# Performance work log

Measured on AMD Instinct MI355X. Metric: run time of the kernel, lower is better.

## Reference

```python
import jax, jax.numpy as jnp
import numpy as np

NUM_NODES = 50000
NUM_HYPEREDGES = 10000
NUM_INCIDENCES = 800000
CHANNELS = 256
NEG_SLOPE = 0.01  # torch leaky_relu default negative_slope


def setup_inputs() -> dict:
    key = jax.random.key(0)
    k_n, k_e, k_emb, k_cw, k_lw, k_lb = jax.random.split(key, 6)
    node_idx = jax.random.randint(k_n, (NUM_INCIDENCES,), 0, NUM_NODES, dtype=jnp.int32)
    edge_idx = jax.random.randint(k_e, (NUM_INCIDENCES,), 0, NUM_HYPEREDGES, dtype=jnp.int32)
    edge_index = jnp.stack([node_idx, edge_idx], axis=0)  # [2, nnz] incidence list
    s = 1.0 / np.sqrt(CHANNELS).astype(np.float32)
    emb = jax.random.normal(k_emb, (NUM_NODES, CHANNELS), jnp.float32)  # Node2Vec embedding table
    conv_w = jax.random.normal(k_cw, (CHANNELS, CHANNELS), jnp.float32) * s  # HypergraphConv.lin (no bias)
    conv_b = jnp.zeros((CHANNELS,), jnp.float32)  # HypergraphConv.bias
    lin_w = jax.random.normal(k_lw, (CHANNELS, CHANNELS), jnp.float32) * s
    lin_b = jax.random.normal(k_lb, (CHANNELS,), jnp.float32) * s
    return {"emb": emb, "conv_w": conv_w, "conv_b": conv_b,
            "lin_w": lin_w, "lin_b": lin_b, "edge_index": edge_index}


def reference(emb, conv_w, conv_b, lin_w, lin_b, edge_index):
    node_idx, edge_idx = edge_index[0], edge_index[1]
    # HypergraphConv (use_attention=False): X' = D^-1 H B^-1 H^T (X W^T) + b
    x = emb @ conv_w.T  # [N, C]
    ones = jnp.ones((NUM_INCIDENCES,), x.dtype)
    D = jax.ops.segment_sum(ones, node_idx, num_segments=NUM_NODES)       # node degree
    Dinv = jnp.where(D > 0, 1.0 / D, 0.0)
    B = jax.ops.segment_sum(ones, edge_idx, num_segments=NUM_HYPEREDGES)  # hyperedge degree
    Binv = jnp.where(B > 0, 1.0 / B, 0.0)
    # node -> hyperedge aggregation
    e = jax.ops.segment_sum(x[node_idx], edge_idx, num_segments=NUM_HYPEREDGES) * Binv[:, None]  # [E, C]
    # hyperedge -> node aggregation
    n = jax.ops.segment_sum(e[edge_idx], node_idx, num_segments=NUM_NODES) * Dinv[:, None] + conv_b  # [N, C]
    y = jax.nn.leaky_relu(n, NEG_SLOPE)
    g = y.T @ y  # [C, C] Gram
    out = jax.nn.leaky_relu(g @ lin_w.T + lin_b, NEG_SLOPE)
    return out
```

## Files before the change

### kernel.cpp

```cpp
#include <hip/hip_runtime.h>

#define N_NODES 50000
#define N_EDGES 10000
#define NNZ     800000
#define C       256
#define SLOPE   0.01f
#define KTOT    50176
#define KCHUNK  512
#define NZB     98
#define MPAD    10048
#define NHALF   25000

#define NB      250
#define EB_E    40
#define EB_N    200
#define CHUNK   3125
#define CAP     6000
#define MP_E    288
#define MP_N    1408

#define EAGG_G  314
#define NAGG_G  1568

#define OFF_CC_E    0
#define OFF_CC_N    1024
#define OFF_CUR_E   2048
#define OFF_CUR_N   3072
#define OFF_DEG_E   4096
#define OFF_DEG_N   45056
#define ZERO_BYTES  245760
#define OFF_CB_E    266240
#define OFF_CB_N    267264
#define OFF_RS_N    268288
#define OFF_RS_E    468480
#define OFF_BUF_E   508672
#define OFF_BUF_N   3708672
#define OFF_CSR_E   6908672
#define OFF_CSR_N   10108672
#define OFF_EMBH    13308672
#define OFF_YT      13308672
#define OFF_E2      44144640
#define OFF_CWH     49289216
#define OFF_PART    49420288
#define OFF_EACCP   OFF_PART

typedef __attribute__((ext_vector_type(8))) short short8;
typedef __attribute__((ext_vector_type(4))) float floatx4;

static __device__ __forceinline__ unsigned short f2bf(float f) {
    unsigned int u = __float_as_uint(f);
    u = (u + 0x7fffu + ((u >> 16) & 1u)) >> 16;
    return (unsigned short)u;
}

static __device__ __forceinline__ void acc_bf8(const uint4 d, float* a) {
    a[0] += __uint_as_float(d.x << 16);
    a[1] += __uint_as_float(d.x & 0xffff0000u);
    a[2] += __uint_as_float(d.y << 16);
    a[3] += __uint_as_float(d.y & 0xffff0000u);
    a[4] += __uint_as_float(d.z << 16);
    a[5] += __uint_as_float(d.z & 0xffff0000u);
    a[6] += __uint_as_float(d.w << 16);
    a[7] += __uint_as_float(d.w & 0xffff0000u);
}

static __device__ __forceinline__ void idx8(const uint4 pk, int* ix) {
    ix[0] = (int)(pk.x & 0xffffu); ix[1] = (int)(pk.x >> 16);
    ix[2] = (int)(pk.y & 0xffffu); ix[3] = (int)(pk.y >> 16);
    ix[4] = (int)(pk.z & 0xffffu); ix[5] = (int)(pk.z >> 16);
    ix[6] = (int)(pk.w & 0xffffu); ix[7] = (int)(pk.w >> 16);
}

static __device__ __forceinline__ unsigned bfadd2(unsigned x, unsigned y) {
    float lx = __uint_as_float(x << 16), hx = __uint_as_float(x & 0xffff0000u);
    float ly = __uint_as_float(y << 16), hy = __uint_as_float(y & 0xffff0000u);
    return (unsigned)f2bf(lx + ly) | ((unsigned)f2bf(hx + hy) << 16);
}
static __device__ __forceinline__ uint4 bfadd8(uint4 x, uint4 y) {
    x.x = bfadd2(x.x, y.x); x.y = bfadd2(x.y, y.y);
    x.z = bfadd2(x.z, y.z); x.w = bfadd2(x.w, y.w);
    return x;
}

__global__ __launch_bounds__(256) void zero_kernel(float4* __restrict__ p, int n4) {
    int i = blockIdx.x * 256 + threadIdx.x;
    if (i < n4) p[i] = make_float4(0.f, 0.f, 0.f, 0.f);
}

#define PREP_EMB_BLOCKS 6251
#define PREP_CW_BLOCKS  32
__global__ __launch_bounds__(256) void prep_kernel(const float4* __restrict__ emb4,
                                                   uint4* __restrict__ embh4,
                                                   const float4* __restrict__ cw4,
                                                   uint4* __restrict__ cwh4,
                                                   const int* __restrict__ node_idx,
                                                   const int* __restrict__ edge_idx,
                                                   int* __restrict__ cc_e,
                                                   int* __restrict__ cc_n) {
    __shared__ int he[NB], hn[NB];
    int b = blockIdx.x, tid = threadIdx.x;
    if (b < PREP_EMB_BLOCKS) {
        int i = b * 256 + tid;
        if (i >= 1600032) return;
        uint4 o = {0u, 0u, 0u, 0u};
        if (i < 1600000) {
            float4 f0 = emb4[2 * i], f1 = emb4[2 * i + 1];
            o.x = f2bf(f0.x) | ((unsigned)f2bf(f0.y) << 16);
            o.y = f2bf(f0.z) | ((unsigned)f2bf(f0.w) << 16);
            o.z = f2bf(f1.x) | ((unsigned)f2bf(f1.y) << 16);
            o.w = f2bf(f1.z) | ((unsigned)f2bf(f1.w) << 16);
        }
        int node = i >> 5, c = i & 31;
        embh4[((size_t)(c >> 3) * 50001 + node) * 8 + (c & 7)] = o;
    } else if (b < PREP_EMB_BLOCKS + PREP_CW_BLOCKS) {
        int i = (b - PREP_EMB_BLOCKS) * 256 + tid;
        float4 f0 = cw4[2 * i], f1 = cw4[2 * i + 1];
        uint4 o;
        o.x = f2bf(f0.x) | ((unsigned)f2bf(f0.y) << 16);
        o.y = f2bf(f0.z) | ((unsigned)f2bf(f0.w) << 16);
        o.z = f2bf(f1.x) | ((unsigned)f2bf(f1.y) << 16);
        o.w = f2bf(f1.z) | ((unsigned)f2bf(f1.w) << 16);
        cwh4[i] = o;
    } else {
        int base = (b - PREP_EMB_BLOCKS - PREP_CW_BLOCKS) * CHUNK;
        for (int i = tid; i < NB; i += 256) { he[i] = 0; hn[i] = 0; }
        __syncthreads();
        for (int i = tid; i < CHUNK; i += 256) {
            atomicAdd(&he[edge_idx[base + i] / EB_E], 1);
            atomicAdd(&hn[node_idx[base + i] / EB_N], 1);
        }
        __syncthreads();
        for (int k = tid; k < NB; k += 256) {
            if (he[k]) atomicAdd(&cc_e[k], he[k]);
            if (hn[k]) atomicAdd(&cc_n[k], hn[k]);
        }
    }
}

__global__ __launch_bounds__(256) void coarse_scan_kernel(const int* __restrict__ cc_e,
                                                          const int* __restrict__ cc_n,
                                                          int* __restrict__ cb_e,
                                                          int* __restrict__ cb_n) {
    __shared__ int tmp[256];
    int tid = threadIdx.x;
    int v = (tid < NB) ? cc_e[tid] : 0;
    tmp[tid] = v;
    __syncthreads();
    for (int off = 1; off < 256; off <<= 1) {
        int t = (tid >= off) ? tmp[tid - off] : 0;
        __syncthreads();
        tmp[tid] += t;
        __syncthreads();
    }
    if (tid < NB) cb_e[tid + 1] = tmp[tid];
    if (tid == 0) cb_e[0] = 0;
    __syncthreads();
    v = (tid < NB) ? cc_n[tid] : 0;
    tmp[tid] = v;
    __syncthreads();
    for (int off = 1; off < 256; off <<= 1) {
        int t = (tid >= off) ? tmp[tid - off] : 0;
        __syncthreads();
        tmp[tid] += t;
        __syncthreads();
    }
    if (tid < NB) cb_n[tid + 1] = tmp[tid];
    if (tid == 0) cb_n[0] = 0;
}

__global__ __launch_bounds__(256) void bucket_scatter_kernel(const int* __restrict__ node_idx,
                                                             const int* __restrict__ edge_idx,
                                                             const int* __restrict__ cb_e,
                                                             const int* __restrict__ cb_n,
                                                             int* __restrict__ cur_e,
                                                             int* __restrict__ cur_n,
                                                             int* __restrict__ buf_e,
                                                             int* __restrict__ buf_n) {
    __shared__ int he[NB], hn[NB], be[NB], bn[NB];
    int tid = threadIdx.x;
    int base = blockIdx.x * CHUNK;
    for (int i = tid; i < NB; i += 256) { he[i] = 0; hn[i] = 0; }
    __syncthreads();
    int pe[13], pn[13];
    #pragma unroll
    for (int k = 0; k < 13; k++) {
        int i = tid + k * 256;
        if (i < CHUNK) {
            int e = edge_idx[base + i], v = node_idx[base + i];
            int ke = e / EB_E, kn = v / EB_N;
            pe[k] = (ke << 12) | atomicAdd(&he[ke], 1);
            pn[k] = (kn << 12) | atomicAdd(&hn[kn], 1);
        }
    }
    __syncthreads();
    for (int k = tid; k < NB; k += 256) {
        int c = he[k];
        be[k] = cb_e[k] + (c ? atomicAdd(&cur_e[k], c) : 0);
        int cn = hn[k];
        bn[k] = cb_n[k] + (cn ? atomicAdd(&cur_n[k], cn) : 0);
    }
    __syncthreads();
    #pragma unroll
    for (int k = 0; k < 13; k++) {
        int i = tid + k * 256;
        if (i < CHUNK) {
            int e = edge_idx[base + i], v = node_idx[base + i];
            int ke = pe[k] >> 12, oe = pe[k] & 4095;
            buf_e[be[ke] + oe] = (v << 6) | (e - ke * EB_E);
            int kn = pn[k] >> 12, on = pn[k] & 4095;
            buf_n[bn[kn] + on] = (e << 8) | (v - kn * EB_N);
        }
    }
}

__global__ __launch_bounds__(256) void bucket_sort_kernel(const int* __restrict__ buf_e,
                                                          const int* __restrict__ buf_n,
                                                          const int* __restrict__ cb_e,
                                                          const int* __restrict__ cb_n,
                                                          unsigned short* __restrict__ csr_e,
                                                          unsigned short* __restrict__ csr_n,
                                                          int* __restrict__ rs_e,
                                                          int* __restrict__ rs_n,
                                                          int* __restrict__ deg_e,
                                                          int* __restrict__ deg_n) {
    __shared__ int A[CAP];
    __shared__ int h[EB_N], bs[EB_N], cs[EB_N];
    int tid = threadIdx.x;
    bool edgeSide = blockIdx.x < NB;
    int k = edgeSide ? blockIdx.x : blockIdx.x - NB;
    int eb = edgeSide ? EB_E : EB_N;
    int shift = edgeSide ? 6 : 8;
    int mask = (1 << shift) - 1;
    int mp = edgeSide ? MP_E : MP_N;
    int sent = edgeSide ? N_NODES : N_EDGES;
    const int* cb  = edgeSide ? cb_e : cb_n;
    const int* buf = edgeSide ? buf_e : buf_n;
    unsigned short* csr = edgeSide ? csr_e : csr_n;
    int* rs  = edgeSide ? rs_e : rs_n;
    int* deg = edgeSide ? deg_e : deg_n;
    int base = cb[k];
    int base_pad = (base + k * mp + 7) & ~7;
    int cnt = cb[k + 1] - base;
    for (int i = tid; i < eb; i += 256) h[i] = 0;
    __syncthreads();
    for (int i = tid; i < cnt; i += 256) {
        int it = buf[base + i];
        if (i < CAP) A[i] = it;
        atomicAdd(&h[it & mask], 1);
    }
    __syncthreads();
    if (tid == 0) {
        int s = 0;
        for (int j = 0; j < eb; j++) { bs[j] = s; s += (h[j] + 7) & ~7; }
    }
    __syncthreads();
    for (int j = tid; j < eb; j += 256) {
        rs[k * eb + j] = base_pad + bs[j];
        deg[k * eb + j] = h[j];
        cs[j] = h[j];
        h[j] = 0;
    }
    if (tid == 0 && k == NB - 1) rs[edgeSide ? N_EDGES : N_NODES] = NNZ;
    __syncthreads();
    for (int j = tid; j < eb; j += 256) {
        int c0 = cs[j], e0 = (c0 + 7) & ~7;
        for (int x = c0; x < e0; x++) csr[base_pad + bs[j] + x] = (unsigned short)sent;
    }
    for (int i = tid; i < cnt; i += 256) {
        int it = (i < CAP) ? A[i] : buf[base + i];
        int loc = it & mask;
        int off = bs[loc] + atomicAdd(&h[loc], 1);
        csr[base_pad + off] = (unsigned short)(it >> shift);
    }
}

__global__ __launch_bounds__(256) void edge_aggregate_kernel(const uint4* __restrict__ embh4,
                                                             const unsigned short* __restrict__ csr_e,
                                                             const int* __restrict__ rs_e,
                                                             const int* __restrict__ deg_e,
                                                             unsigned short* __restrict__ e_accp) {
    int sid = blockIdx.x & 7, g = blockIdx.x >> 3;
    int cslice = sid & 3, half = sid >> 2;
    int lo = half * NHALF, hi = lo + NHALF;
    const uint4* __restrict__ csr4 = (const uint4*)csr_e;
    int tid = threadIdx.x;
    int group = tid >> 3, l8 = tid & 7;
    const uint4* __restrict__ tbl = embh4 + (size_t)cslice * 50001 * 8 + l8;
    int e = g * 32 + group;
    int s = rs_e[min(e, N_EDGES)];
    int dg = deg_e[e];
    int c0 = s >> 3, nc = (dg + 7) >> 3;
    float a[8] = {0.f, 0.f, 0.f, 0.f, 0.f, 0.f, 0.f, 0.f};
    for (int c = c0; c < c0 + nc; c++) {
        uint4 pk = csr4[c];
        int ix[8];
        idx8(pk, ix);
        #pragma unroll
        for (int j = 0; j < 8; j++) {
            int v = ix[j];
            if (v >= lo && v < hi)
                acc_bf8(tbl[(size_t)v * 8], a);
        }
    }
    uint4 o;
    o.x = f2bf(a[0]) | ((unsigned)f2bf(a[1]) << 16);
    o.y = f2bf(a[2]) | ((unsigned)f2bf(a[3]) << 16);
    o.z = f2bf(a[4]) | ((unsigned)f2bf(a[5]) << 16);
    o.w = f2bf(a[6]) | ((unsigned)f2bf(a[7]) << 16);
    *(uint4*)(e_accp + ((size_t)half * MPAD + e) * C + cslice * 64 + l8 * 8) = o;
}

__global__ __launch_bounds__(256) void edge_gemm_mfma_kernel(const unsigned short* __restrict__ e_accp,
                                                             const unsigned short* __restrict__ cwh,
                                                             const int* __restrict__ deg_e,
                                                             unsigned short* __restrict__ e2h) {
    __shared__ __align__(16) unsigned short As[64 * 72];
    __shared__ __align__(16) unsigned short Bs[64 * 72];
    int i0 = blockIdx.x * 64, j0 = blockIdx.y * 64;
    int tid = threadIdx.x;
    int w = tid >> 6, lane = tid & 63;
    int col = lane & 15, quad = lane >> 4;
    floatx4 acc[4] = {};
    for (int step = 0; step < 4; step++) {
        int kb = step * 64;
        __syncthreads();
        #pragma unroll
        for (int l = 0; l < 2; l++) {
            int slot = tid + l * 256;
            int row = slot >> 3, grp = slot & 7;
            uint4 d0 = *(const uint4*)(e_accp + (size_t)(i0 + row) * C + kb + grp * 8);
            uint4 d1 = *(const uint4*)(e_accp + ((size_t)MPAD + i0 + row) * C + kb + grp * 8);
            *(uint4*)(&As[row * 72 + grp * 8]) = bfadd8(d0, d1);
            uint4 db = *(const uint4*)(cwh + (size_t)(j0 + row) * C + kb + grp * 8);
            *(uint4*)(&Bs[row * 72 + grp * 8]) = db;
        }
        __syncthreads();
        #pragma unroll
        for (int sub = 0; sub < 2; sub++) {
            short8 a = *(const short8*)(&As[(w * 16 + col) * 72 + sub * 32 + quad * 8]);
            #pragma unroll
            for (int jt = 0; jt < 4; jt++) {
                short8 b = *(const short8*)(&Bs[(jt * 16 + col) * 72 + sub * 32 + quad * 8]);
                acc[jt] = __builtin_amdgcn_mfma_f32_16x16x32_bf16(a, b, acc[jt], 0, 0, 0);
            }
        }
    }
    #pragma unroll
    for (int r = 0; r < 4; r++) {
        int m = i0 + w * 16 + quad * 4 + r;
        int dg = deg_e[m];
        float binv = (dg > 0) ? 1.0f / (float)dg : 0.0f;
        #pragma unroll
        for (int jt = 0; jt < 4; jt++) {
            int ch = j0 + jt * 16 + col;
            e2h[(size_t)((ch >> 6) * MPAD + m) * 64 + (ch & 63)] = f2bf(acc[jt][r] * binv);
        }
    }
}

__global__ __launch_bounds__(256) void node_aggregate_t_kernel(const uint4* __restrict__ e2h4,
                                                               const unsigned short* __restrict__ csr_n,
                                                               const int* __restrict__ rs_n,
                                                               const int* __restrict__ deg_n,
                                                               const float* __restrict__ conv_b,
                                                               unsigned short* __restrict__ yT) {
    __shared__ unsigned short T[64][33];
    int sid = blockIdx.x & 3, g = blockIdx.x >> 2;
    const uint4* __restrict__ csr4 = (const uint4*)csr_n;
    int tid = threadIdx.x;
    int group = tid >> 3, l8 = tid & 7;
    const uint4* __restrict__ tbl = e2h4 + (size_t)sid * MPAD * 8 + l8;
    int n = g * 32 + group;
    int s = rs_n[min(n, N_NODES)];
    int dg = deg_n[n];
    int c0 = s >> 3, nc = (dg + 7) >> 3;
    float4 b0 = ((const float4*)conv_b)[sid * 16 + l8 * 2];
    float4 b1 = ((const float4*)conv_b)[sid * 16 + l8 * 2 + 1];
    float a[8] = {0.f, 0.f, 0.f, 0.f, 0.f, 0.f, 0.f, 0.f};
    for (int c = c0; c < c0 + nc; c++) {
        uint4 pk = csr4[c];
        int ix[8];
        idx8(pk, ix);
        #pragma unroll
        for (int j = 0; j < 8; j++) acc_bf8(tbl[(size_t)ix[j] * 8], a);
    }
    float dinv = (dg > 0) ? 1.0f / (float)dg : 0.0f;
    float bb[8] = {b0.x, b0.y, b0.z, b0.w, b1.x, b1.y, b1.z, b1.w};
    #pragma unroll
    for (int jj = 0; jj < 8; jj++) {
        float r = a[jj] * dinv + bb[jj];
        r = (r > 0.f) ? r : SLOPE * r;
        if (n >= N_NODES) r = 0.f;
        T[l8 * 8 + jj][group] = f2bf(r);
    }
    __syncthreads();
    int rr = tid >> 2, cc = tid & 3;
    uint4 o;
    o.x = T[rr][cc * 8 + 0] | ((unsigned)T[rr][cc * 8 + 1] << 16);
    o.y = T[rr][cc * 8 + 2] | ((unsigned)T[rr][cc * 8 + 3] << 16);
    o.z = T[rr][cc * 8 + 4] | ((unsigned)T[rr][cc * 8 + 5] << 16);
    o.w = T[rr][cc * 8 + 6] | ((unsigned)T[rr][cc * 8 + 7] << 16);
    *(uint4*)(yT + (size_t)(sid * 64 + rr) * KTOT + g * 32 + cc * 8) = o;
}

__global__ __launch_bounds__(256) void gram_mfma_kernel(const unsigned short* __restrict__ yT,
                                                        float* __restrict__ part) {
    static const int PI[10] = {0, 0, 0, 0, 1, 1, 1, 2, 2, 3};
    static const int PJ[10] = {0, 1, 2, 3, 1, 2, 3, 2, 3, 3};
    __shared__ __align__(16) unsigned short As[64 * 72];
    __shared__ __align__(16) unsigned short Bs[64 * 72];
    int i0 = PI[blockIdx.x] * 64, j0 = PJ[blockIdx.x] * 64;
    bool diag = (i0 == j0);
    int kb0 = blockIdx.y * KCHUNK;
    int tid = threadIdx.x;
    int w = tid >> 6, lane = tid & 63;
    int col = lane & 15, quad = lane >> 4;
    floatx4 acc[4] = {};
    for (int step = 0; step < KCHUNK / 64; step++) {
        int kb = kb0 + step * 64;
        __syncthreads();
        #pragma unroll
        for (int l = 0; l < 2; l++) {
            int slot = tid + l * 256;
            int row = slot >> 3, grp = slot & 7;
            uint4 da = *(const uint4*)(yT + (size_t)(i0 + row) * KTOT + kb + grp * 8);
            *(uint4*)(&As[row * 72 + grp * 8]) = da;
            if (!diag) {
                uint4 db = *(const uint4*)(yT + (size_t)(j0 + row) * KTOT + kb + grp * 8);
                *(uint4*)(&Bs[row * 72 + grp * 8]) = db;
            }
        }
        __syncthreads();
        const unsigned short* Bb = diag ? As : Bs;
        #pragma unroll
        for (int sub = 0; sub < 2; sub++) {
            short8 a = *(const short8*)(&As[(w * 16 + col) * 72 + sub * 32 + quad * 8]);
            #pragma unroll
            for (int jt = 0; jt < 4; jt++) {
                short8 b = *(const short8*)(&Bb[(jt * 16 + col) * 72 + sub * 32 + quad * 8]);
                acc[jt] = __builtin_amdgcn_mfma_f32_16x16x32_bf16(a, b, acc[jt], 0, 0, 0);
            }
        }
    }
    float* slab = part + ((size_t)blockIdx.y * 10 + blockIdx.x) * 4096;
    #pragma unroll
    for (int jt = 0; jt < 4; jt++)
        #pragma unroll
        for (int r = 0; r < 4; r++)
            slab[(w * 16 + quad * 4 + r) * 64 + jt * 16 + col] = acc[jt][r];
}

__global__ __launch_bounds__(256) void greduce_out_kernel(const float* __restrict__ part,
                                                          const float* __restrict__ lin_w,
                                                          const float* __restrict__ lin_b,
                                                          float* __restrict__ out) {
    __shared__ float gs[C];
    int i = blockIdx.x, j = threadIdx.x;
    int a = i >> 6, b = j >> 6;
    int lo = min(a, b), hi = max(a, b);
    int t = lo * (7 - lo) / 2 + hi;
    int li = (a <= b) ? (i & 63) : (j & 63);
    int lj = (a <= b) ? (j & 63) : (i & 63);
    const float* p = part + (size_t)t * 4096 + li * 64 + lj;
    float s = 0.f;
    for (int z = 0; z < NZB; z++) s += p[(size_t)z * 40960];
    gs[j] = s;
    __syncthreads();
    float acc = lin_b[j];
    const float* wrow = lin_w + (size_t)j * C;
    for (int k = 0; k < C; k++) acc += gs[k] * wrow[k];
    out[(size_t)i * C + j] = (acc > 0.f) ? acc : SLOPE * acc;
}

extern "C" void kernel_launch(void* const* d_in, const int* in_sizes, int n_in,
                              void* d_out, int out_size, void* d_ws, size_t ws_size,
                              hipStream_t stream) {
    const float* emb    = (const float*)d_in[0];
    const float* conv_w = (const float*)d_in[1];
    const float* conv_b = (const float*)d_in[2];
    const float* lin_w  = (const float*)d_in[3];
    const float* lin_b  = (const float*)d_in[4];
    const int*   eidx   = (const int*)d_in[5];
    const int* node_idx = eidx;
    const int* edge_idx = eidx + NNZ;

    char* ws = (char*)d_ws;
    int* cc_e  = (int*)(ws + OFF_CC_E);
    int* cc_n  = (int*)(ws + OFF_CC_N);
    int* cur_e = (int*)(ws + OFF_CUR_E);
    int* cur_n = (int*)(ws + OFF_CUR_N);
    int* deg_e = (int*)(ws + OFF_DEG_E);
    int* deg_n = (int*)(ws + OFF_DEG_N);
    int* cb_e  = (int*)(ws + OFF_CB_E);
    int* cb_n  = (int*)(ws + OFF_CB_N);
    int* rs_n  = (int*)(ws + OFF_RS_N);
    int* rs_e  = (int*)(ws + OFF_RS_E);
    int* buf_e = (int*)(ws + OFF_BUF_E);
    int* buf_n = (int*)(ws + OFF_BUF_N);
    unsigned short* csr_e = (unsigned short*)(ws + OFF_CSR_E);
    unsigned short* csr_n = (unsigned short*)(ws + OFF_CSR_N);
    uint4* embh4 = (uint4*)(ws + OFF_EMBH);
    unsigned short* e_accp = (unsigned short*)(ws + OFF_EACCP);
    unsigned short* e2h = (unsigned short*)(ws + OFF_E2);
    unsigned short* cwh = (unsigned short*)(ws + OFF_CWH);
    unsigned short* yT  = (unsigned short*)(ws + OFF_YT);
    float* part = (float*)(ws + OFF_PART);
    float* out = (float*)d_out;

    zero_kernel<<<ZERO_BYTES / 4096, 256, 0, stream>>>((float4*)ws, ZERO_BYTES / 16);

    prep_kernel<<<PREP_EMB_BLOCKS + PREP_CW_BLOCKS + 256, 256, 0, stream>>>(
        (const float4*)emb, embh4, (const float4*)conv_w, (uint4*)cwh,
        node_idx, edge_idx, cc_e, cc_n);

    coarse_scan_kernel<<<1, 256, 0, stream>>>(cc_e, cc_n, cb_e, cb_n);

    bucket_scatter_kernel<<<256, 256, 0, stream>>>(node_idx, edge_idx, cb_e, cb_n,
                                                   cur_e, cur_n, buf_e, buf_n);

    bucket_sort_kernel<<<2 * NB, 256, 0, stream>>>(buf_e, buf_n, cb_e, cb_n,
                                                   csr_e, csr_n, rs_e, rs_n,
                                                   deg_e, deg_n);

    edge_aggregate_kernel<<<8 * EAGG_G, 256, 0, stream>>>(embh4, csr_e, rs_e, deg_e, e_accp);

    edge_gemm_mfma_kernel<<<dim3(MPAD / 64, C / 64), 256, 0, stream>>>(e_accp, cwh, deg_e, e2h);

    node_aggregate_t_kernel<<<4 * NAGG_G, 256, 0, stream>>>((const uint4*)e2h, csr_n, rs_n,
                                                            deg_n, conv_b, yT);

    gram_mfma_kernel<<<dim3(10, NZB), 256, 0, stream>>>(yT, part);

    greduce_out_kernel<<<C, 256, 0, stream>>>(part, lin_w, lin_b, out);
}
```

Measured before the change: 299.3 us.

## Pre-split edge CSR rows by node half to skip filtered gathers

The edge-side bucket sort now bins each incidence by (edge, node-half), so every hyperedge row holds two padded sub-lists with separate degree arrays. The edge aggregation blocks for each half then walk only their own sub-list instead of scanning the whole row and discarding out-of-range nodes, which roughly halves the index loads and branch work. Degree arrays are now written explicitly, including the padding tail, so the zeroing kernel shrinks to one block. The cost is more padding in the edge CSR, since each row now pads two sub-lists, and a slightly more complex sort.

```diff
diff --git a/kernel.cpp b/kernel.cpp
--- a/kernel.cpp
+++ b/kernel.cpp
@@ -16,7 +16,7 @@
 #define EB_N    200
 #define CHUNK   3125
 #define CAP     6000
-#define MP_E    288
+#define MP_E    576
 #define MP_N    1408
 
 #define EAGG_G  314
@@ -26,17 +26,18 @@
 #define OFF_CC_N    1024
 #define OFF_CUR_E   2048
 #define OFF_CUR_N   3072
-#define OFF_DEG_E   4096
-#define OFF_DEG_N   45056
-#define ZERO_BYTES  245760
-#define OFF_CB_E    266240
-#define OFF_CB_N    267264
-#define OFF_RS_N    268288
-#define OFF_RS_E    468480
-#define OFF_BUF_E   508672
-#define OFF_BUF_N   3708672
-#define OFF_CSR_E   6908672
-#define OFF_CSR_N   10108672
+#define ZERO_BYTES  4096
+#define OFF_DEG_E0  4096
+#define OFF_DEG_E1  45056
+#define OFF_DEG_N   86016
+#define OFF_CB_E    286720
+#define OFF_CB_N    288768
+#define OFF_RS_N    290816
+#define OFF_RS_E    491520
+#define OFF_BUF_E   532480
+#define OFF_BUF_N   3732480
+#define OFF_CSR_E   6932480
+#define OFF_CSR_N   8820480
 #define OFF_EMBH    13308672
 #define OFF_YT      13308672
 #define OFF_E2      44144640
@@ -206,7 +207,7 @@
         if (i < CHUNK) {
             int e = edge_idx[base + i], v = node_idx[base + i];
             int ke = pe[k] >> 12, oe = pe[k] & 4095;
-            buf_e[be[ke] + oe] = (v << 6) | (e - ke * EB_E);
+            buf_e[be[ke] + oe] = (v << 7) | ((e - ke * EB_E) * 2 + (v >= NHALF ? 1 : 0));
             int kn = pn[k] >> 12, on = pn[k] & 4095;
             buf_n[bn[kn] + on] = (e << 8) | (v - kn * EB_N);
         }
@@ -221,15 +222,17 @@
                                                           unsigned short* __restrict__ csr_n,
                                                           int* __restrict__ rs_e,
                                                           int* __restrict__ rs_n,
-                                                          int* __restrict__ deg_e,
+                                                          int* __restrict__ deg_e0,
+                                                          int* __restrict__ deg_e1,
                                                           int* __restrict__ deg_n) {
     __shared__ int A[CAP];
     __shared__ int h[EB_N], bs[EB_N], cs[EB_N];
     int tid = threadIdx.x;
     bool edgeSide = blockIdx.x < NB;
     int k = edgeSide ? blockIdx.x : blockIdx.x - NB;
-    int eb = edgeSide ? EB_E : EB_N;
-    int shift = edgeSide ? 6 : 8;
+    int rows = edgeSide ? EB_E : EB_N;
+    int bins = edgeSide ? 2 * EB_E : EB_N;
+    int shift = edgeSide ? 7 : 8;
     int mask = (1 << shift) - 1;
     int mp = edgeSide ? MP_E : MP_N;
     int sent = edgeSide ? N_NODES : N_EDGES;
@@ -237,11 +240,10 @@
     const int* buf = edgeSide ? buf_e : buf_n;
     unsigned short* csr = edgeSide ? csr_e : csr_n;
     int* rs  = edgeSide ? rs_e : rs_n;
-    int* deg = edgeSide ? deg_e : deg_n;
     int base = cb[k];
     int base_pad = (base + k * mp + 7) & ~7;
     int cnt = cb[k + 1] - base;
-    for (int i = tid; i < eb; i += 256) h[i] = 0;
+    for (int i = tid; i < bins; i += 256) h[i] = 0;
     __syncthreads();
     for (int i = tid; i < cnt; i += 256) {
         int it = buf[base + i];
@@ -251,18 +253,31 @@
     __syncthreads();
     if (tid == 0) {
         int s = 0;
-        for (int j = 0; j < eb; j++) { bs[j] = s; s += (h[j] + 7) & ~7; }
-    }
-    __syncthreads();
-    for (int j = tid; j < eb; j += 256) {
-        rs[k * eb + j] = base_pad + bs[j];
-        deg[k * eb + j] = h[j];
-        cs[j] = h[j];
-        h[j] = 0;
-    }
-    if (tid == 0 && k == NB - 1) rs[edgeSide ? N_EDGES : N_NODES] = NNZ;
-    __syncthreads();
-    for (int j = tid; j < eb; j += 256) {
+        for (int j = 0; j < bins; j++) { bs[j] = s; s += (h[j] + 7) & ~7; }
+    }
+    __syncthreads();
+    for (int j = tid; j < bins; j += 256) { cs[j] = h[j]; h[j] = 0; }
+    __syncthreads();
+    for (int j = tid; j < rows; j += 256) {
+        if (edgeSide) {
+            rs[k * EB_E + j] = base_pad + bs[2 * j];
+            deg_e0[k * EB_E + j] = cs[2 * j];
+            deg_e1[k * EB_E + j] = cs[2 * j + 1];
+        } else {
+            rs[k * EB_N + j] = base_pad + bs[j];
+            deg_n[k * EB_N + j] = cs[j];
+        }
+    }
+    if (k == NB - 1) {
+        if (tid == 0) rs[edgeSide ? N_EDGES : N_NODES] = NNZ;
+        if (edgeSide) {
+            if (tid < MPAD - N_EDGES) { deg_e0[N_EDGES + tid] = 0; deg_e1[N_EDGES + tid] = 0; }
+        } else {
+            for (int x = tid; x < KTOT - N_NODES; x += 256) deg_n[N_NODES + x] = 0;
+        }
+    }
+    __syncthreads();
+    for (int j = tid; j < bins; j += 256) {
         int c0 = cs[j], e0 = (c0 + 7) & ~7;
         for (int x = c0; x < e0; x++) csr[base_pad + bs[j] + x] = (unsigned short)sent;
     }
@@ -277,30 +292,28 @@
 __global__ __launch_bounds__(256) void edge_aggregate_kernel(const uint4* __restrict__ embh4,
                                                              const unsigned short* __restrict__ csr_e,
                                                              const int* __restrict__ rs_e,
-                                                             const int* __restrict__ deg_e,
+                                                             const int* __restrict__ deg_e0,
+                                                             const int* __restrict__ deg_e1,
                                                              unsigned short* __restrict__ e_accp) {
     int sid = blockIdx.x & 7, g = blockIdx.x >> 3;
     int cslice = sid & 3, half = sid >> 2;
-    int lo = half * NHALF, hi = lo + NHALF;
     const uint4* __restrict__ csr4 = (const uint4*)csr_e;
     int tid = threadIdx.x;
     int group = tid >> 3, l8 = tid & 7;
     const uint4* __restrict__ tbl = embh4 + (size_t)cslice * 50001 * 8 + l8;
     int e = g * 32 + group;
     int s = rs_e[min(e, N_EDGES)];
-    int dg = deg_e[e];
-    int c0 = s >> 3, nc = (dg + 7) >> 3;
+    int d0 = deg_e0[e], d1 = deg_e1[e];
+    int start = half ? s + ((d0 + 7) & ~7) : s;
+    int dgh = half ? d1 : d0;
+    int c0 = start >> 3, nc = (dgh + 7) >> 3;
     float a[8] = {0.f, 0.f, 0.f, 0.f, 0.f, 0.f, 0.f, 0.f};
     for (int c = c0; c < c0 + nc; c++) {
         uint4 pk = csr4[c];
         int ix[8];
         idx8(pk, ix);
         #pragma unroll
-        for (int j = 0; j < 8; j++) {
-            int v = ix[j];
-            if (v >= lo && v < hi)
-                acc_bf8(tbl[(size_t)v * 8], a);
-        }
+        for (int j = 0; j < 8; j++) acc_bf8(tbl[(size_t)ix[j] * 8], a);
     }
     uint4 o;
     o.x = f2bf(a[0]) | ((unsigned)f2bf(a[1]) << 16);
@@ -312,7 +325,8 @@
 
 __global__ __launch_bounds__(256) void edge_gemm_mfma_kernel(const unsigned short* __restrict__ e_accp,
                                                              const unsigned short* __restrict__ cwh,
-                                                             const int* __restrict__ deg_e,
+                                                             const int* __restrict__ deg_e0,
+                                                             const int* __restrict__ deg_e1,
                                                              unsigned short* __restrict__ e2h) {
     __shared__ __align__(16) unsigned short As[64 * 72];
     __shared__ __align__(16) unsigned short Bs[64 * 72];
@@ -348,7 +362,7 @@
     #pragma unroll
     for (int r = 0; r < 4; r++) {
         int m = i0 + w * 16 + quad * 4 + r;
-        int dg = deg_e[m];
+        int dg = deg_e0[m] + deg_e1[m];
         float binv = (dg > 0) ? 1.0f / (float)dg : 0.0f;
         #pragma unroll
         for (int jt = 0; jt < 4; jt++) {
@@ -489,7 +503,8 @@
     int* cc_n  = (int*)(ws + OFF_CC_N);
     int* cur_e = (int*)(ws + OFF_CUR_E);
     int* cur_n = (int*)(ws + OFF_CUR_N);
-    int* deg_e = (int*)(ws + OFF_DEG_E);
+    int* deg_e0 = (int*)(ws + OFF_DEG_E0);
+    int* deg_e1 = (int*)(ws + OFF_DEG_E1);
     int* deg_n = (int*)(ws + OFF_DEG_N);
     int* cb_e  = (int*)(ws + OFF_CB_E);
     int* cb_n  = (int*)(ws + OFF_CB_N);
@@ -507,7 +522,7 @@
     float* part = (float*)(ws + OFF_PART);
     float* out = (float*)d_out;
 
-    zero_kernel<<<ZERO_BYTES / 4096, 256, 0, stream>>>((float4*)ws, ZERO_BYTES / 16);
+    zero_kernel<<<1, 256, 0, stream>>>((float4*)ws, ZERO_BYTES / 16);
 
     prep_kernel<<<PREP_EMB_BLOCKS + PREP_CW_BLOCKS + 256, 256, 0, stream>>>(
         (const float4*)emb, embh4, (const float4*)conv_w, (uint4*)cwh,
@@ -520,11 +535,13 @@
 
     bucket_sort_kernel<<<2 * NB, 256, 0, stream>>>(buf_e, buf_n, cb_e, cb_n,
                                                    csr_e, csr_n, rs_e, rs_n,
-                                                   deg_e, deg_n);
-
-    edge_aggregate_kernel<<<8 * EAGG_G, 256, 0, stream>>>(embh4, csr_e, rs_e, deg_e, e_accp);
-
-    edge_gemm_mfma_kernel<<<dim3(MPAD / 64, C / 64), 256, 0, stream>>>(e_accp, cwh, deg_e, e2h);
+                                                   deg_e0, deg_e1, deg_n);
+
+    edge_aggregate_kernel<<<8 * EAGG_G, 256, 0, stream>>>(embh4, csr_e, rs_e,
+                                                          deg_e0, deg_e1, e_accp);
+
+    edge_gemm_mfma_kernel<<<dim3(MPAD / 64, C / 64), 256, 0, stream>>>(e_accp, cwh,
+                                                                       deg_e0, deg_e1, e2h);
 
     node_aggregate_t_kernel<<<4 * NAGG_G, 256, 0, stream>>>((const uint4*)e2h, csr_n, rs_n,
                                                             deg_n, conv_b, yT);
```

After: 258.7 us. 1.16x faster.
